# Performance work log

Hardware: AMD Instinct MI355X
Metric: run time of the kernel (lower is better)

## Reference

```python
import jax, jax.numpy as jnp
import numpy as np

N_EMBED = 8192
BETA = 0.25


def setup_inputs() -> dict:
    key = jax.random.key(0)
    k1, k2 = jax.random.split(key)
    z = jax.random.normal(k1, (16, 256, 32, 32), dtype=jnp.float32)
    # matches nn.Embedding init uniform_(-1/n_embed, 1/n_embed)
    embed_weight = jax.random.uniform(k2, (N_EMBED, 256), dtype=jnp.float32,
                                      minval=-1.0 / N_EMBED, maxval=1.0 / N_EMBED)
    return {"z": z, "embed_weight": embed_weight}


def reference(z, embed_weight):
    sg = jax.lax.stop_gradient
    # b c h w -> b h w c
    z_nhwc = jnp.transpose(z, (0, 2, 3, 1))
    # squared L2 distance to every code: ||z||^2 + ||e||^2 - 2 z.e  -> [b,h,w,n]
    d = (jnp.sum(z_nhwc ** 2, axis=-1, keepdims=True)
         + jnp.sum(embed_weight ** 2, axis=1)
         - 2.0 * jnp.einsum('bhwc,nc->bhwn', z_nhwc, embed_weight))
    indices = jnp.argmin(d, axis=-1)            # [b,h,w] int
    z_q = embed_weight[indices]                  # [b,h,w,c] gather

    loss = (BETA * jnp.mean((sg(z_q) - z_nhwc) ** 2)
            + jnp.mean((z_q - sg(z_nhwc)) ** 2))

    # straight-through estimator
    z_q_st = z_nhwc + sg(z_q - z_nhwc)
    out = jnp.transpose(z_q_st, (0, 3, 1, 2))    # b h w c -> b c h w

    # perplexity via histogram (equivalent to one_hot(...).mean(0))
    flat = indices.reshape(-1)
    counts = jnp.zeros((N_EMBED,), dtype=jnp.float32).at[flat].add(1.0)
    avg_probs = counts / flat.shape[0]
    perplexity = jnp.exp(-jnp.sum(avg_probs * jnp.log(avg_probs + 1e-10)))

    return (out, indices, loss, perplexity)
```

## Files before the change

kernel.cpp:

```cpp
#include <hip/hip_runtime.h>
#include <stdint.h>

typedef unsigned long long u64;
typedef unsigned int u32;

#define CDIM 256
#define NCODES 8192
#define MTOT 16384
#define OUT_ELEMS 4194304
#define BETA 0.25f

#define WS_PACKED 0u
#define WS_ENORM  131072u
#define WS_ZSQ    163840u
#define WS_COUNTS 229376u
#define WS_LOSS   262144u
#define WS_ZSQ4   262400u
#define WS_ZB     524544u
#define WS_EB     8913152u
#define WS_TT2    13107456u
#define WS_NEEDED 21496064u

typedef short bf16x8 __attribute__((ext_vector_type(8)));
typedef float f32x4 __attribute__((ext_vector_type(4)));

#define GL2LDS16(g, l) __builtin_amdgcn_global_load_lds(            \
    (const __attribute__((address_space(1))) void*)(g),             \
    (__attribute__((address_space(3))) void*)(l), 16, 0, 0)

__device__ __forceinline__ unsigned short f2bf(float f) {
  u32 u = __float_as_uint(f);
  u32 r = (u + 0x7FFFu + ((u >> 16) & 1u)) >> 16;
  return (unsigned short)r;
}

__global__ void conv_kernel(const float* __restrict__ z, const float* __restrict__ E,
                            unsigned short* __restrict__ zb, unsigned short* __restrict__ eb,
                            float* __restrict__ zsq4, float* __restrict__ enorm) {
  int blk = blockIdx.x;
  int t = threadIdx.x, w = t >> 6, lane = t & 63;
  if (blk < 1024) {
    __shared__ unsigned short tz[64][66];
    __shared__ float part[4][64];
    int b = blk >> 6, rem = blk & 63;
    int ct = rem >> 4, pt = rem & 15;
    int c0 = ct << 6, p0 = pt << 6;
    const float* zp = z + ((size_t)b << 18) + ((size_t)c0 << 10) + p0;
    float sq = 0.f;
    #pragma unroll
    for (int i = 0; i < 16; ++i) {
      int cl = w + (i << 2);
      float v = zp[((size_t)cl << 10) + lane];
      sq = fmaf(v, v, sq);
      tz[cl][lane] = f2bf(v);
    }
    part[w][lane] = sq;
    __syncthreads();
    if (w == 0) {
      float s = ((part[0][lane] + part[1][lane]) + part[2][lane]) + part[3][lane];
      zsq4[(((size_t)b << 10) + p0 + lane) * 4 + ct] = s;
    }
    #pragma unroll
    for (int j = 0; j < 16; ++j) {
      int pl = w + (j << 2);
      zb[(((size_t)b << 10) + p0 + pl) * 256 + c0 + lane] = tz[lane][pl];
    }
  } else {
    int e4 = blk - 1024;
    size_t base = ((size_t)e4 << 11) + ((size_t)t << 3);
    float4 v0 = *(const float4*)&E[base];
    float4 v1 = *(const float4*)&E[base + 4];
    ushort4 o0 = { f2bf(v0.x), f2bf(v0.y), f2bf(v0.z), f2bf(v0.w) };
    ushort4 o1 = { f2bf(v1.x), f2bf(v1.y), f2bf(v1.z), f2bf(v1.w) };
    *(ushort4*)&eb[base] = o0;
    *(ushort4*)&eb[base + 4] = o1;
    float s = v0.x * v0.x + v0.y * v0.y + v0.z * v0.z + v0.w * v0.w
            + v1.x * v1.x + v1.y * v1.y + v1.z * v1.z + v1.w * v1.w;
    #pragma unroll
    for (int off = 16; off; off >>= 1) s += __shfl_xor(s, off, 32);
    if ((t & 31) == 0) enorm[(e4 << 3) + (t >> 5)] = s;
  }
}

__global__ void zsqfin_kernel(const float* __restrict__ zsq4, float* __restrict__ zsq) {
  int m = blockIdx.x * 256 + threadIdx.x;
  float4 v = *(const float4*)&zsq4[(size_t)m * 4];
  zsq[m] = ((v.x + v.y) + v.z) + v.w;
}

__global__ __launch_bounds__(256, 2) void gemm_kernel(
    const unsigned short* __restrict__ zb, const unsigned short* __restrict__ eb,
    uint2* __restrict__ tt2) {
  __shared__ unsigned short As[256 * 64];
  __shared__ unsigned short Bs[128 * 64];
  const int t = threadIdx.x;
  const int w = t >> 6, lane = t & 63;
  const int r16 = lane & 15, kg = lane >> 4, r7 = r16 & 7;

  const int lin = ((int)blockIdx.y << 6) + (int)blockIdx.x;
  const int xk = lin & 7, loc = lin >> 3;
  const int bx = ((xk & 3) << 4) | (loc & 15);
  const int by = ((xk >> 2) << 5) | (loc >> 4);
  const int m0 = bx << 8, n0 = by << 7;

  f32x4 acc[4][8];
  #pragma unroll
  for (int i = 0; i < 4; ++i)
    #pragma unroll
    for (int j = 0; j < 8; ++j) acc[i][j] = (f32x4)0.f;

  const int jsw = ((t & 7) ^ ((t >> 3) & 7)) << 3;
  const unsigned short* zsrc = zb + (((size_t)m0 + (t >> 3)) << 8) + jsw;
  const unsigned short* esrc = eb + (((size_t)n0 + (t >> 3)) << 8) + jsw;

  const int jx0 = (kg ^ r7) << 4;
  const int jx1 = ((4 + kg) ^ r7) << 4;
  const int arow = ((w << 6) + r16) << 7;
  const int brow = r16 << 7;

  for (int kt = 0; kt < 4; ++kt) {
    if (kt) __syncthreads();
    const int ko = kt << 6;
    #pragma unroll
    for (int i = 0; i < 8; ++i)
      GL2LDS16(zsrc + (i << 13) + ko, (char*)As + (i << 12) + (t << 4));
    #pragma unroll
    for (int i = 0; i < 4; ++i)
      GL2LDS16(esrc + (i << 13) + ko, (char*)Bs + (i << 12) + (t << 4));
    __syncthreads();
    #pragma unroll
    for (int s = 0; s < 2; ++s) {
      const int jx = s ? jx1 : jx0;
      bf16x8 af[4], bq[8];
      #pragma unroll
      for (int mi = 0; mi < 4; ++mi)
        af[mi] = *(const bf16x8*)((const char*)As + arow + (mi << 11) + jx);
      #pragma unroll
      for (int ni = 0; ni < 8; ++ni)
        bq[ni] = *(const bf16x8*)((const char*)Bs + brow + (ni << 11) + jx);
      #pragma unroll
      for (int mi = 0; mi < 4; ++mi)
        #pragma unroll
        for (int ni = 0; ni < 8; ++ni)
          acc[mi][ni] = __builtin_amdgcn_mfma_f32_16x16x32_bf16(bq[ni], af[mi], acc[mi][ni], 0, 0, 0);
    }
  }

  const u32 kgr = (u32)(kg << 2);
  #pragma unroll
  for (int mi = 0; mi < 4; ++mi) {
    float a1 = 0.f, a2 = 0.f;
    #pragma unroll
    for (int ni = 0; ni < 8; ++ni) {
      #pragma unroll
      for (int reg = 0; reg < 4; ++reg) {
        u32 e = __float_as_uint(acc[mi][ni][reg] + 2.0f);
        float k = __uint_as_float((e & 0xFFFFFF80u) | ((u32)(ni << 4) | kgr | (u32)reg));
        float na2 = __builtin_amdgcn_fmed3f(a1, a2, k);
        a1 = fmaxf(a1, k);
        a2 = na2;
      }
    }
    #pragma unroll
    for (int off = 16; off < 64; off <<= 1) {
      float b1 = __shfl_xor(a1, off, 64);
      float b2 = __shfl_xor(a2, off, 64);
      a2 = fmaxf(fminf(a1, b1), fmaxf(a2, b2));
      a1 = fmaxf(a1, b1);
    }
    if (kg == 0) {
      int row = m0 + (w << 6) + (mi << 4) + r16;
      tt2[((size_t)by << 14) + row] =
          make_uint2(__float_as_uint(a1), __float_as_uint(a2));
    }
  }
}

__global__ __launch_bounds__(256) void refine_out_kernel(
    const float* __restrict__ z, const float* __restrict__ E,
    const float* __restrict__ zsq, const float* __restrict__ enorm,
    const uint2* __restrict__ tt2, u64* __restrict__ packed,
    float* __restrict__ out, float* __restrict__ out_idx,
    u32* __restrict__ counts, float* __restrict__ loss_acc) {
  __shared__ uint2 tc[64][33];
  __shared__ float zrow[32][260];
  __shared__ float red[4];
  const int t = threadIdx.x, w = t >> 6, lane = t & 63;
  const int m0 = blockIdx.x << 5;
  const int b = m0 >> 10, p0 = m0 & 1023;

  #pragma unroll
  for (int i = 0; i < 8; ++i) {
    int tau = (i << 3) + (t >> 5);
    tc[tau][t & 31] = tt2[((size_t)tau << 14) + m0 + (t & 31)];
  }
  #pragma unroll
  for (int i = 0; i < 8; ++i) {
    int c = (i << 5) + (t >> 3);
    int p4 = (t & 7) << 2;
    float4 v = *(const float4*)&z[((size_t)b << 18) + ((size_t)c << 10) + p0 + p4];
    zrow[p4 + 0][c] = v.x;
    zrow[p4 + 1][c] = v.y;
    zrow[p4 + 2][c] = v.z;
    zrow[p4 + 3][c] = v.w;
  }
  __syncthreads();

  float wloss = 0.f;
  for (int j = 0; j < 8; ++j) {
    const int rr = (w << 3) + j;
    const int m = m0 + rr;
    uint2 c = tc[lane][rr];
    float f0 = __uint_as_float(c.x), f1 = __uint_as_float(c.y);
    float fm = f0;
    #pragma unroll
    for (int off = 1; off < 64; off <<= 1) fm = fmaxf(fm, __shfl_xor(fm, off, 64));
    float thr = fm - 1.5e-4f;
    const float4 zr4 = *(const float4*)&zrow[rr][lane << 2];
    float zsqm = zsq[m];
    u64 best = ~0ull;
    float4 be4 = {0.f, 0.f, 0.f, 0.f};
    #pragma unroll
    for (int s = 0; s < 2; ++s) {
      u32 ck = s ? c.y : c.x;
      float fv = s ? f1 : f0;
      u64 mask = __ballot(fv >= thr);
      while (mask) {
        int src = __ffsll((unsigned long long)mask) - 1;
        mask &= mask - 1;
        u32 key = (u32)__shfl((int)ck, src, 64);
        int idx = (src << 7) | (int)(key & 127u);
        const float4 e4 = *(const float4*)&E[(size_t)idx * CDIM + (lane << 2)];
        float pa = zr4.x * e4.x;
        pa = fmaf(zr4.y, e4.y, pa);
        pa = fmaf(zr4.z, e4.z, pa);
        pa = fmaf(zr4.w, e4.w, pa);
        #pragma unroll
        for (int off = 1; off < 64; off <<= 1) pa += __shfl_xor(pa, off, 64);
        float ttv = zsqm + enorm[idx];
        float d = ttv - 2.0f * pa;
        u64 k2 = ((u64)__float_as_uint(d) << 32) | (u32)idx;
        bool better = k2 < best;
        best = better ? k2 : best;
        be4 = better ? e4 : be4;
      }
    }
    float4 df, o4;
    df.x = be4.x - zr4.x; df.y = be4.y - zr4.y; df.z = be4.z - zr4.z; df.w = be4.w - zr4.w;
    o4.x = zr4.x + df.x;  o4.y = zr4.y + df.y;  o4.z = zr4.z + df.z;  o4.w = zr4.w + df.w;
    wloss = fmaf(df.x, df.x, wloss);
    wloss = fmaf(df.y, df.y, wloss);
    wloss = fmaf(df.z, df.z, wloss);
    wloss = fmaf(df.w, df.w, wloss);
    *(float4*)&zrow[rr][lane << 2] = o4;
    if (lane == 0) {
      packed[m] = best;
      int idx = (int)(u32)(best & 0xffffffffull);
      out_idx[m] = (float)idx;
      atomicAdd(&counts[idx], 1u);
    }
  }
  #pragma unroll
  for (int off = 32; off; off >>= 1) wloss += __shfl_down(wloss, off, 64);
  if (lane == 0) red[w] = wloss;
  __syncthreads();
  if (t == 0) atomicAdd(loss_acc, red[0] + red[1] + red[2] + red[3]);

  #pragma unroll
  for (int i = 0; i < 8; ++i) {
    int c = (i << 5) + (t >> 3);
    int p4 = (t & 7) << 2;
    float4 o = { zrow[p4 + 0][c], zrow[p4 + 1][c], zrow[p4 + 2][c], zrow[p4 + 3][c] };
    *(float4*)&out[((size_t)b << 18) + ((size_t)c << 10) + p0 + p4] = o;
  }
}

__global__ void enorm_kernel(const float* __restrict__ E, float* __restrict__ enorm) {
  int wave = threadIdx.x >> 6;
  int lane = threadIdx.x & 63;
  int n = blockIdx.x * 4 + wave;
  float4 v = reinterpret_cast<const float4*>(E + (size_t)n * CDIM)[lane];
  float s = v.x * v.x + v.y * v.y + v.z * v.z + v.w * v.w;
  #pragma unroll
  for (int off = 32; off; off >>= 1) s += __shfl_down(s, off, 64);
  if (lane == 0) enorm[n] = s;
}

__global__ void zsq_kernel(const float* __restrict__ z, float* __restrict__ zsq) {
  int blk = blockIdx.x;
  int j = threadIdx.x;
  int b = blk >> 2;
  int p = ((blk & 3) << 8) + j;
  const float* zp = z + (size_t)b * (CDIM * 1024) + p;
  float acc = 0.f;
  #pragma unroll 8
  for (int c = 0; c < CDIM; ++c) {
    float v = zp[(size_t)c * 1024];
    acc += v * v;
  }
  zsq[(blk << 8) + j] = acc;
}

#define BM 128
#define BN 128
#define BK 32
__global__ __launch_bounds__(256, 2) void dist_kernel(
    const float* __restrict__ z, const float* __restrict__ E,
    const float* __restrict__ zsq, const float* __restrict__ enorm,
    unsigned long long* __restrict__ packed) {
  __shared__ float zs[BK][BM];
  __shared__ float es[BK][BN];
  const int t = threadIdx.x;
  const int m0 = blockIdx.x * BM;
  const int n0 = blockIdx.y * BN;
  const int b = m0 >> 10;
  const int p0 = m0 & 1023;
  const int zc = t >> 5;
  const int zm = (t & 31) << 2;
  const float* zbase = z + (size_t)b * 262144 + p0 + zm;
  const int en = t & 127;
  const int ec = (t >> 7) << 4;
  const float* ebase = E + (size_t)(n0 + en) * CDIM + ec;
  float4 zr[4], er[4];
  #pragma unroll
  for (int r = 0; r < 4; ++r)
    zr[r] = *(const float4*)(zbase + (size_t)(r * 8 + zc) * 1024);
  #pragma unroll
  for (int i = 0; i < 4; ++i)
    er[i] = *(const float4*)(ebase + 4 * i);
  float acc[8][8];
  #pragma unroll
  for (int a = 0; a < 8; ++a)
    #pragma unroll
    for (int bb = 0; bb < 8; ++bb) acc[a][bb] = 0.f;
  const int tx = t & 15, ty = t >> 4;
  for (int kt = 0; kt < CDIM / BK; ++kt) {
    __syncthreads();
    #pragma unroll
    for (int r = 0; r < 4; ++r)
      *(float4*)&zs[r * 8 + zc][zm] = zr[r];
    #pragma unroll
    for (int i = 0; i < 4; ++i) {
      es[ec + 4 * i + 0][en] = er[i].x;
      es[ec + 4 * i + 1][en] = er[i].y;
      es[ec + 4 * i + 2][en] = er[i].z;
      es[ec + 4 * i + 3][en] = er[i].w;
    }
    __syncthreads();
    if (kt + 1 < CDIM / BK) {
      const int c0 = (kt + 1) * BK;
      #pragma unroll
      for (int r = 0; r < 4; ++r)
        zr[r] = *(const float4*)(zbase + (size_t)(c0 + r * 8 + zc) * 1024);
      #pragma unroll
      for (int i = 0; i < 4; ++i)
        er[i] = *(const float4*)(ebase + c0 + 4 * i);
    }
    #pragma unroll 8
    for (int kk = 0; kk < BK; ++kk) {
      float4 za = *(const float4*)&zs[kk][ty * 4];
      float4 zb4 = *(const float4*)&zs[kk][64 + ty * 4];
      float4 ea = *(const float4*)&es[kk][tx * 4];
      float4 eb4 = *(const float4*)&es[kk][64 + tx * 4];
      float zv[8] = {za.x, za.y, za.z, za.w, zb4.x, zb4.y, zb4.z, zb4.w};
      float ev[8] = {ea.x, ea.y, ea.z, ea.w, eb4.x, eb4.y, eb4.z, eb4.w};
      #pragma unroll
      for (int a = 0; a < 8; ++a)
        #pragma unroll
        for (int bb = 0; bb < 8; ++bb)
          acc[a][bb] += zv[a] * ev[bb];
    }
  }
  #pragma unroll
  for (int a = 0; a < 8; ++a) {
    int rloc = (a < 4) ? (ty * 4 + a) : (64 + ty * 4 + (a - 4));
    float zq = zsq[m0 + rloc];
    float bestd = 3.4e38f;
    int bestn = 0;
    #pragma unroll
    for (int bb = 0; bb < 8; ++bb) {
      int nloc = (bb < 4) ? (tx * 4 + bb) : (64 + tx * 4 + (bb - 4));
      int n = n0 + nloc;
      float ttv = zq + enorm[n];
      float d = ttv - 2.0f * acc[a][bb];
      if (d < bestd) { bestd = d; bestn = n; }
    }
    unsigned long long pk =
        ((unsigned long long)__float_as_uint(bestd) << 32) | (unsigned)bestn;
    #pragma unroll
    for (int off = 1; off < 16; off <<= 1) {
      unsigned long long other = __shfl_xor(pk, off, 16);
      if (other < pk) pk = other;
    }
    if (tx == 0) atomicMin(&packed[m0 + rloc], pk);
  }
}

__global__ void idx_kernel(const unsigned long long* __restrict__ packed,
                           float* __restrict__ out_idx, unsigned int* __restrict__ counts) {
  int m = blockIdx.x * 256 + threadIdx.x;
  int idx = (int)(unsigned)(packed[m] & 0xffffffffull);
  out_idx[m] = (float)idx;
  atomicAdd(&counts[idx], 1u);
}

__global__ __launch_bounds__(256) void out_kernel(
    const float* __restrict__ z, const float* __restrict__ E,
    const u64* __restrict__ packed,
    float* __restrict__ out, float* __restrict__ loss_acc) {
  __shared__ float es[32][257];
  const int t = threadIdx.x, w = t >> 6, lane = t & 63;
  const int m0 = blockIdx.x << 5;
  const int b = m0 >> 10, p0 = m0 & 1023;
  #pragma unroll
  for (int i = 0; i < 8; ++i) {
    int pl = (w << 3) + i;
    int idx = (int)(u32)(packed[m0 + pl] & 0xffffffffull);
    float4 v = *(const float4*)&E[((size_t)idx << 8) + (lane << 2)];
    es[pl][(lane << 2) + 0] = v.x;
    es[pl][(lane << 2) + 1] = v.y;
    es[pl][(lane << 2) + 2] = v.z;
    es[pl][(lane << 2) + 3] = v.w;
  }
  __syncthreads();
  const int pp = lane & 31, chi = lane >> 5;
  const size_t gbase = ((size_t)b << 18) + p0 + pp;
  float s = 0.f;
  #pragma unroll 8
  for (int i = 0; i < 32; ++i) {
    int c = (i << 3) + (w << 1) + chi;
    float zv = z[gbase + ((size_t)c << 10)];
    float e = es[pp][c];
    float diff = e - zv;
    out[gbase + ((size_t)c << 10)] = zv + diff;
    s = fmaf(diff, diff, s);
  }
  #pragma unroll
  for (int off = 32; off; off >>= 1) s += __shfl_down(s, off, 64);
  __shared__ float red[4];
  if (lane == 0) red[w] = s;
  __syncthreads();
  if (t == 0) atomicAdd(loss_acc, red[0] + red[1] + red[2] + red[3]);
}

__global__ void scalar_kernel(const unsigned int* __restrict__ counts,
                              const float* __restrict__ loss_acc,
                              float* __restrict__ out) {
  float s = 0.f;
  for (int i = threadIdx.x; i < NCODES; i += 256) {
    float pl = (float)counts[i] * (1.0f / 16384.0f);
    s += pl * logf(pl + 1e-10f);
  }
  #pragma unroll
  for (int off = 32; off; off >>= 1) s += __shfl_down(s, off, 64);
  __shared__ float red[4];
  int wv = threadIdx.x >> 6, lane = threadIdx.x & 63;
  if (lane == 0) red[wv] = s;
  __syncthreads();
  if (threadIdx.x == 0) {
    float tot = red[0] + red[1] + red[2] + red[3];
    out[OUT_ELEMS + MTOT] = (1.0f + BETA) * loss_acc[0] * (1.0f / (float)OUT_ELEMS);
    out[OUT_ELEMS + MTOT + 1] = expf(-tot);
  }
}

extern "C" void kernel_launch(void* const* d_in, const int* in_sizes, int n_in,
                              void* d_out, int out_size, void* d_ws, size_t ws_size,
                              hipStream_t stream) {
  const float* z = (const float*)d_in[0];
  const float* E = (const float*)d_in[1];
  float* out = (float*)d_out;
  char* ws = (char*)d_ws;
  u64* packed = (u64*)(ws + WS_PACKED);
  float* enorm = (float*)(ws + WS_ENORM);
  float* zsq = (float*)(ws + WS_ZSQ);
  u32* counts = (u32*)(ws + WS_COUNTS);
  float* loss_acc = (float*)(ws + WS_LOSS);

  hipMemsetAsync(counts, 0, 32768 + 256, stream);

  if (ws_size >= WS_NEEDED) {
    unsigned short* zb = (unsigned short*)(ws + WS_ZB);
    unsigned short* ebuf = (unsigned short*)(ws + WS_EB);
    uint2* tt2 = (uint2*)(ws + WS_TT2);
    float* zsq4 = (float*)(ws + WS_ZSQ4);
    conv_kernel<<<2048, 256, 0, stream>>>(z, E, zb, ebuf, zsq4, enorm);
    zsqfin_kernel<<<64, 256, 0, stream>>>(zsq4, zsq);
    dim3 g(MTOT / 256, NCODES / 128);
    gemm_kernel<<<g, 256, 0, stream>>>(zb, ebuf, tt2);
    refine_out_kernel<<<MTOT / 32, 256, 0, stream>>>(z, E, zsq, enorm, tt2, packed,
                                                     out, out + OUT_ELEMS, counts, loss_acc);
  } else {
    hipMemsetAsync(packed, 0xFF, MTOT * 8, stream);
    enorm_kernel<<<NCODES / 4, 256, 0, stream>>>(E, enorm);
    zsq_kernel<<<64, 256, 0, stream>>>(z, zsq);
    dim3 g(MTOT / BM, NCODES / BN);
    dist_kernel<<<g, 256, 0, stream>>>(z, E, zsq, enorm, packed);
    idx_kernel<<<MTOT / 256, 256, 0, stream>>>(packed, out + OUT_ELEMS, counts);
    out_kernel<<<MTOT / 32, 256, 0, stream>>>(z, E, packed, out, loss_acc);
  }

  scalar_kernel<<<1, 256, 0, stream>>>(counts, loss_acc, out);
}
```

Before: 146.2 us.

## Double-buffer GEMM LDS tiles with K=32 stages and drop block swizzle

```diff
diff --git a/kernel.cpp b/kernel.cpp
--- a/kernel.cpp
+++ b/kernel.cpp
@@ -88,20 +88,15 @@
   zsq[m] = ((v.x + v.y) + v.z) + v.w;
 }
 
-__global__ __launch_bounds__(256, 2) void gemm_kernel(
+__global__ __launch_bounds__(256, 3) void gemm_kernel(
     const unsigned short* __restrict__ zb, const unsigned short* __restrict__ eb,
     uint2* __restrict__ tt2) {
-  __shared__ unsigned short As[256 * 64];
-  __shared__ unsigned short Bs[128 * 64];
+  __shared__ unsigned short As[2][256 * 32];
+  __shared__ unsigned short Bs[2][128 * 32];
   const int t = threadIdx.x;
   const int w = t >> 6, lane = t & 63;
-  const int r16 = lane & 15, kg = lane >> 4, r7 = r16 & 7;
-
-  const int lin = ((int)blockIdx.y << 6) + (int)blockIdx.x;
-  const int xk = lin & 7, loc = lin >> 3;
-  const int bx = ((xk & 3) << 4) | (loc & 15);
-  const int by = ((xk >> 2) << 5) | (loc >> 4);
-  const int m0 = bx << 8, n0 = by << 7;
+  const int r16 = lane & 15, kg = lane >> 4;
+  const int m0 = blockIdx.x << 8, n0 = blockIdx.y << 7;
 
   f32x4 acc[4][8];
   #pragma unroll
@@ -109,41 +104,47 @@
     #pragma unroll
     for (int j = 0; j < 8; ++j) acc[i][j] = (f32x4)0.f;
 
-  const int jsw = ((t & 7) ^ ((t >> 3) & 7)) << 3;
-  const unsigned short* zsrc = zb + (((size_t)m0 + (t >> 3)) << 8) + jsw;
-  const unsigned short* esrc = eb + (((size_t)n0 + (t >> 3)) << 8) + jsw;
-
-  const int jx0 = (kg ^ r7) << 4;
-  const int jx1 = ((4 + kg) ^ r7) << 4;
-  const int arow = ((w << 6) + r16) << 7;
-  const int brow = r16 << 7;
-
-  for (int kt = 0; kt < 4; ++kt) {
-    if (kt) __syncthreads();
-    const int ko = kt << 6;
-    #pragma unroll
-    for (int i = 0; i < 8; ++i)
-      GL2LDS16(zsrc + (i << 13) + ko, (char*)As + (i << 12) + (t << 4));
-    #pragma unroll
-    for (int i = 0; i < 4; ++i)
-      GL2LDS16(esrc + (i << 13) + ko, (char*)Bs + (i << 12) + (t << 4));
+  const int jsw = ((t & 3) ^ ((t >> 3) & 3)) << 3;
+  const unsigned short* zsrc = zb + (((size_t)m0 + (t >> 2)) << 8) + jsw;
+  const unsigned short* esrc = eb + (((size_t)n0 + (t >> 2)) << 8) + jsw;
+
+  const int jx = (kg ^ ((r16 >> 1) & 3)) << 4;
+  const int arow = ((w << 6) + r16) << 6;
+  const int brow = r16 << 6;
+
+  #pragma unroll
+  for (int i = 0; i < 4; ++i)
+    GL2LDS16(zsrc + (i << 14), (char*)As[0] + (i << 12) + (t << 4));
+  #pragma unroll
+  for (int i = 0; i < 2; ++i)
+    GL2LDS16(esrc + (i << 14), (char*)Bs[0] + (i << 12) + (t << 4));
+  __syncthreads();
+
+  #pragma unroll
+  for (int kt = 0; kt < 8; ++kt) {
+    const int cur = kt & 1;
+    if (kt < 7) {
+      const int ko = (kt + 1) << 5;
+      #pragma unroll
+      for (int i = 0; i < 4; ++i)
+        GL2LDS16(zsrc + (i << 14) + ko, (char*)As[cur ^ 1] + (i << 12) + (t << 4));
+      #pragma unroll
+      for (int i = 0; i < 2; ++i)
+        GL2LDS16(esrc + (i << 14) + ko, (char*)Bs[cur ^ 1] + (i << 12) + (t << 4));
+    }
+    bf16x8 af[4], bq[8];
+    #pragma unroll
+    for (int mi = 0; mi < 4; ++mi)
+      af[mi] = *(const bf16x8*)((const char*)As[cur] + arow + (mi << 10) + jx);
+    #pragma unroll
+    for (int ni = 0; ni < 8; ++ni)
+      bq[ni] = *(const bf16x8*)((const char*)Bs[cur] + brow + (ni << 10) + jx);
+    #pragma unroll
+    for (int mi = 0; mi < 4; ++mi)
+      #pragma unroll
+      for (int ni = 0; ni < 8; ++ni)
+        acc[mi][ni] = __builtin_amdgcn_mfma_f32_16x16x32_bf16(bq[ni], af[mi], acc[mi][ni], 0, 0, 0);
     __syncthreads();
-    #pragma unroll
-    for (int s = 0; s < 2; ++s) {
-      const int jx = s ? jx1 : jx0;
-      bf16x8 af[4], bq[8];
-      #pragma unroll
-      for (int mi = 0; mi < 4; ++mi)
-        af[mi] = *(const bf16x8*)((const char*)As + arow + (mi << 11) + jx);
-      #pragma unroll
-      for (int ni = 0; ni < 8; ++ni)
-        bq[ni] = *(const bf16x8*)((const char*)Bs + brow + (ni << 11) + jx);
-      #pragma unroll
-      for (int mi = 0; mi < 4; ++mi)
-        #pragma unroll
-        for (int ni = 0; ni < 8; ++ni)
-          acc[mi][ni] = __builtin_amdgcn_mfma_f32_16x16x32_bf16(bq[ni], af[mi], acc[mi][ni], 0, 0, 0);
-    }
   }
 
   const u32 kgr = (u32)(kg << 2);
@@ -170,7 +171,7 @@
     }
     if (kg == 0) {
       int row = m0 + (w << 6) + (mi << 4) + r16;
-      tt2[((size_t)by << 14) + row] =
+      tt2[((size_t)blockIdx.y << 14) + row] =
           make_uint2(__float_as_uint(a1), __float_as_uint(a2));
     }
   }
```

Result: slower. 230.5 us (+57.6%).
